# Optimization experiments

Hardware: AMD Instinct MI355X
Metric: run time of the kernel (lower is better)

The kernel has to match this reference:

```python
import jax, jax.numpy as jnp
import numpy as np

B, T, V, E, U, L = 64, 1024, 512, 256, 512, 3


def setup_inputs() -> dict:
    key = jax.random.key(0)
    ks = jax.random.split(key, 16)
    inp = {}
    inp['tokens'] = jax.random.randint(ks[0], (B, T), 0, V)
    inp['lengths'] = jax.random.randint(ks[1], (B,), 1, T + 1)
    inp['emb'] = jax.random.normal(ks[2], (V, E), jnp.float32) * 0.05
    in_dims = [E, U, U]
    for l in range(L):
        inp[f'Wk{l}'] = jax.random.normal(ks[3 + 3 * l], (in_dims[l], 4 * U), jnp.float32) * 0.05
        inp[f'Wr{l}'] = jax.random.normal(ks[4 + 3 * l], (U, 4 * U), jnp.float32) * 0.05
        # Keras unit_forget_bias: forget-gate bias initialized to 1
        b = jnp.zeros((4 * U,), jnp.float32)
        inp[f'b{l}'] = b.at[U:2 * U].set(1.0)
    inp['Wd'] = jax.random.normal(ks[12], (U, V), jnp.float32) * 0.05
    inp['bd'] = jnp.zeros((V,), jnp.float32)
    return inp


def _lstm_layer(x_tm, mask_tm, Wk, Wr, b):
    # x_tm: [T,B,D] time-major, mask_tm: [T,B] bool
    Bb = x_tm.shape[1]
    Uu = Wr.shape[0]
    h0 = jnp.zeros((Bb, Uu), x_tm.dtype)
    c0 = jnp.zeros((Bb, Uu), x_tm.dtype)

    def step(carry, inp):
        h, c = carry
        xt, mt = inp
        z = xt @ Wk + h @ Wr + b  # [B, 4U]
        i, f, g, o = jnp.split(z, 4, axis=-1)
        i = jax.nn.sigmoid(i)
        f = jax.nn.sigmoid(f)
        g = jnp.tanh(g)
        o = jax.nn.sigmoid(o)
        c_new = f * c + i * g
        h_new = o * jnp.tanh(c_new)
        m = mt[:, None]
        # masked steps: carry previous state, emit zeros (zero_output_for_mask=True)
        h2 = jnp.where(m, h_new, h)
        c2 = jnp.where(m, c_new, c)
        out = jnp.where(m, h_new, jnp.zeros_like(h_new))
        return (h2, c2), out

    _, ys = jax.lax.scan(step, (h0, c0), (x_tm, mask_tm))
    return ys  # [T,B,U]


def reference(tokens, lengths, emb, Wk0, Wr0, b0, Wk1, Wr1, b1, Wk2, Wr2, b2, Wd, bd):
    Tt = tokens.shape[1]
    mask = jnp.arange(Tt)[None, :] < lengths[:, None]  # [B,T], sequence_mask
    x = emb[tokens]  # [B,T,E] embedding lookup
    x = jnp.swapaxes(x, 0, 1)  # time-major [T,B,E]
    m = jnp.swapaxes(mask, 0, 1)  # [T,B]
    for Wk, Wr, b in ((Wk0, Wr0, b0), (Wk1, Wr1, b1), (Wk2, Wr2, b2)):
        x = _lstm_layer(x, m, Wk, Wr, b)
    x = jnp.swapaxes(x, 0, 1)  # [B,T,U]
    logits = x @ Wd + bd  # [B,T,V]
    return logits
```

## Files before the change

kernel.cpp:

```cpp
#include <hip/hip_runtime.h>
#include <stdint.h>

typedef unsigned short u16;
typedef unsigned int   u32;
typedef unsigned long long u64;
typedef _Float16 half8 __attribute__((ext_vector_type(8)));
typedef __attribute__((ext_vector_type(4))) float f32x4;

#define DEV static __device__ __forceinline__

DEV float bf2f(u16 u){ union{u32 i; float f;} v; v.i=((u32)u)<<16; return v.f; }
DEV u16 f2bf(float f){ u32 x=__float_as_uint(f); return (u16)((x + 0x7FFFu + ((x>>16)&1u))>>16); }
DEV u16 f2hu(float f){ _Float16 h = (_Float16)f; return *(u16*)&h; }
DEV float hu2f(u16 u){ _Float16 h = *(_Float16*)&u; return (float)h; }
DEV float sigm(float x){ return 1.0f/(1.0f+__expf(-x)); }
DEV float tanhr(float x){ float a=fabsf(x); float e=__expf(-2.0f*a); float t=(1.0f-e)/(1.0f+e); return x<0.0f? -t:t; }

typedef const __attribute__((address_space(1))) u32 gu32;
typedef __attribute__((address_space(3))) u32 lu32;
DEV void gload16(const void* g, void* l){
  __builtin_amdgcn_global_load_lds((gu32*)g, (lu32*)l, 16, 0, 0);
}
DEV void gstore4c(void* p, u32 v){
  asm volatile("global_store_dword %0, %1, off sc0 sc1" : : "v"(p), "v"(v) : "memory");
}

DEV u16 ld_h(const void* p, size_t i, int isbf){
  float f = isbf ? bf2f(((const u16*)p)[i]) : ((const float*)p)[i];
  return f2hu(f);
}

__global__ void detect_dtype(const void* emb, u32* flag)
{
  const u16* p = (const u16*)emb;
  int i = threadIdx.x;
  u32 e0 = (p[i]    >> 7) & 0xFF;
  u32 e1 = (p[i+64] >> 7) & 0xFF;
  unsigned long long b0 = __ballot(e0 >= 0x60 && e0 <= 0x7E);
  unsigned long long b1 = __ballot(e1 >= 0x60 && e1 <= 0x7E);
  if (i == 0) *flag = (__popcll(b0) + __popcll(b1) > 96) ? 1u : 0u;
}

__global__ __launch_bounds__(256) void embconv(const void* __restrict__ emb, u16* __restrict__ embH,
                                               const u32* __restrict__ flag)
{
  const int isbf = *flag;
  int i = blockIdx.x*256 + threadIdx.x;
  embH[i] = ld_h(emb, i, isbf);
}

__global__ __launch_bounds__(256) void transpose_bt(const void* __restrict__ in,
                                                    u16* __restrict__ out,
                                                    int K, int N, int perm,
                                                    const u32* __restrict__ flag)
{
  const int isbf = *flag;
  __shared__ u16 t[32][33];
  int nb = blockIdx.x*32, kb = blockIdx.y*32;
  int tx = threadIdx.x & 31, ty = threadIdx.x >> 5;
  #pragma unroll
  for (int i=0;i<4;++i){
    int kl = ty + i*8;
    t[kl][tx] = ld_h(in, (size_t)(kb+kl)*N + nb + tx, isbf);
  }
  __syncthreads();
  #pragma unroll
  for (int i=0;i<4;++i){
    int nl = ty + i*8;
    int n = nb + nl;
    int np = perm ? ((n & 511)*4 + (n >> 9)) : n;
    out[(size_t)np*K + kb + tx] = t[tx][nl];
  }
}

__global__ __launch_bounds__(256) void bias_prep(const void* __restrict__ in, float* __restrict__ out,
                                                 int N, int perm, const u32* __restrict__ flag)
{
  const int isbf = *flag;
  int n = blockIdx.x*256 + threadIdx.x;
  if (n < N){
    int np = perm ? ((n & 511)*4 + (n >> 9)) : n;
    out[np] = isbf ? bf2f(((const u16*)in)[n]) : ((const float*)in)[n];
  }
}

__global__ __launch_bounds__(256) void gemm3(
    const u16* __restrict__ A1, const u16* __restrict__ A2,
    const u16* __restrict__ BT0, const u16* __restrict__ BT1, const u16* __restrict__ BT2,
    const float* __restrict__ b0p, const float* __restrict__ b1p, const float* __restrict__ b2p,
    u16* __restrict__ C0, u16* __restrict__ C1, u16* __restrict__ C2,
    const int* __restrict__ tok, const u16* __restrict__ embH, int t0g,
    int act0, int act1, int act2)
{
  const int z = blockIdx.z;
  if (z==0 && !act0) return;
  if (z==1 && !act1) return;
  if (z==2 && !act2) return;
  const int K = (z==0) ? 256 : 512;
  const u16* BT = z==0?BT0 : z==1?BT1 : BT2;
  const float* bias = z==0?b0p : z==1?b1p : b2p;
  u16* C = z==0?C0 : z==1?C1 : C2;

  __shared__ u16 As[128*32];
  __shared__ u16 Bs[128*32];
  const int tid = threadIdx.x, lane = tid & 63, wid = tid >> 6;
  const int wr = wid >> 1, wc = wid & 1;
  const int m0 = blockIdx.x*128, n0 = blockIdx.y*128;
  const int r  = tid >> 2;
  const int ce = (tid & 3)*8;
  const u16 *a0, *a1;
  if (z == 0){
    int r0 = m0 + r;     int tt = t0g + (r0>>6); int bb = r0 & 63;
    a0 = embH + (size_t)tok[bb*1024 + tt]*256 + ce;
    int r1 = m0 + 64 + r; tt = t0g + (r1>>6); bb = r1 & 63;
    a1 = embH + (size_t)tok[bb*1024 + tt]*256 + ce;
  } else {
    const u16* A = (z==1) ? A1 : A2;
    a0 = A + (size_t)(m0 + r)*512 + ce;
    a1 = A + (size_t)(m0 + 64 + r)*512 + ce;
  }
  const u16* bp0 = BT + (size_t)(n0 + r)*K + ce;
  const u16* bp1 = BT + (size_t)(n0 + 64 + r)*K + ce;
  char* asw0 = (char*)As + (wid<<10);
  char* asw1 = (char*)As + 4096 + (wid<<10);
  char* bsw0 = (char*)Bs + (wid<<10);
  char* bsw1 = (char*)Bs + 4096 + (wid<<10);

  f32x4 acc[4][4];
  #pragma unroll
  for (int i=0;i<4;++i)
    #pragma unroll
    for (int j=0;j<4;++j) acc[i][j] = (f32x4){0.f,0.f,0.f,0.f};

  const int koff = (lane>>4)*8;
  for (int k0 = 0; k0 < K; k0 += 32){
    __syncthreads();
    gload16(a0 + k0, asw0);
    gload16(a1 + k0, asw1);
    gload16(bp0 + k0, bsw0);
    gload16(bp1 + k0, bsw1);
    __syncthreads();
    half8 af[4], bf[4];
    #pragma unroll
    for (int mt=0;mt<4;++mt) af[mt] = *(const half8*)(As + (wr*64 + mt*16 + (lane&15))*32 + koff);
    #pragma unroll
    for (int nt=0;nt<4;++nt) bf[nt] = *(const half8*)(Bs + (wc*64 + nt*16 + (lane&15))*32 + koff);
    #pragma unroll
    for (int mt=0;mt<4;++mt)
      #pragma unroll
      for (int nt=0;nt<4;++nt)
        acc[mt][nt] = __builtin_amdgcn_mfma_f32_16x16x32_f16(bf[nt], af[mt], acc[mt][nt], 0,0,0);
  }
  #pragma unroll
  for (int mt=0;mt<4;++mt){
    int m = m0 + wr*64 + mt*16 + (lane&15);
    int ltl = m >> 6, b = m & 63;
    #pragma unroll
    for (int nt=0;nt<4;++nt){
      int u = ((n0 + wc*64 + nt*16) >> 2) + (lane>>4);
      float4 bq = *(const float4*)(bias + u*4);
      u16 qo[4];
      qo[0] = f2hu(acc[mt][nt][0] + bq.x);
      qo[1] = f2hu(acc[mt][nt][1] + bq.y);
      qo[2] = f2hu(acc[mt][nt][2] + bq.z);
      qo[3] = f2hu(acc[mt][nt][3] + bq.w);
      ((uint2*)C)[(size_t)(ltl*512 + u)*64 + b] = *(uint2*)qo;
    }
  }
}

__global__ __launch_bounds__(256) void gemm_bt(const u16* __restrict__ A, const u16* __restrict__ BT,
                                               const float* __restrict__ bias, void* __restrict__ C,
                                               int M, int N, int K, const u32* __restrict__ flag)
{
  __shared__ u16 As[128*32];
  __shared__ u16 Bs[128*32];
  const int tid = threadIdx.x, lane = tid & 63, wid = tid >> 6;
  const int wr = wid >> 1, wc = wid & 1;
  const int m0 = blockIdx.x*128, n0 = blockIdx.y*128;
  const int r  = tid >> 2;
  const int ce = (tid & 3)*8;
  const u16* a0 = A  + (size_t)(m0 + r)*K + ce;
  const u16* a1 = A  + (size_t)(m0 + 64 + r)*K + ce;
  const u16* b0 = BT + (size_t)(n0 + r)*K + ce;
  const u16* b1 = BT + (size_t)(n0 + 64 + r)*K + ce;
  char* asw0 = (char*)As + (wid<<10);
  char* asw1 = (char*)As + 4096 + (wid<<10);
  char* bsw0 = (char*)Bs + (wid<<10);
  char* bsw1 = (char*)Bs + 4096 + (wid<<10);

  f32x4 acc[4][4];
  #pragma unroll
  for (int i=0;i<4;++i)
    #pragma unroll
    for (int j=0;j<4;++j) acc[i][j] = (f32x4){0.f,0.f,0.f,0.f};

  const int koff = (lane>>4)*8;
  for (int k0 = 0; k0 < K; k0 += 32){
    __syncthreads();
    gload16(a0 + k0, asw0);
    gload16(a1 + k0, asw1);
    gload16(b0 + k0, bsw0);
    gload16(b1 + k0, bsw1);
    __syncthreads();
    half8 af[4], bf[4];
    #pragma unroll
    for (int mt=0;mt<4;++mt) af[mt] = *(const half8*)(As + (wr*64 + mt*16 + (lane&15))*32 + koff);
    #pragma unroll
    for (int nt=0;nt<4;++nt) bf[nt] = *(const half8*)(Bs + (wc*64 + nt*16 + (lane&15))*32 + koff);
    #pragma unroll
    for (int mt=0;mt<4;++mt)
      #pragma unroll
      for (int nt=0;nt<4;++nt)
        acc[mt][nt] = __builtin_amdgcn_mfma_f32_16x16x32_f16(af[mt], bf[nt], acc[mt][nt], 0,0,0);
  }
  const int wrf32 = (*flag == 0);
  #pragma unroll
  for (int mt=0;mt<4;++mt){
    #pragma unroll
    for (int nt=0;nt<4;++nt){
      int col = n0 + wc*64 + nt*16 + (lane&15);
      float bv = bias[col];
      #pragma unroll
      for (int j=0;j<4;++j){
        int row = m0 + wr*64 + mt*16 + ((lane>>4)<<2) + j;
        int orow = ((row & 63) << 10) | (row >> 6);
        float v = acc[mt][nt][j] + bv;
        if (wrf32) ((float*)C)[(size_t)orow*N + col] = v;
        else       ((u16*)C)[(size_t)orow*N + col] = f2bf(v);
      }
    }
  }
}

__global__ __launch_bounds__(256,1) void lstm3(
    const uint2* __restrict__ Zq0, const uint2* __restrict__ Zq1, const uint2* __restrict__ Zq2,
    const u16* __restrict__ Wr0T, const u16* __restrict__ Wr1T, const u16* __restrict__ Wr2T,
    const int* __restrict__ lengths,
    u16* __restrict__ xo0, u16* __restrict__ xo1, u16* __restrict__ xf,
    u32* Hbase, float* Cbase, int d)
{
  __shared__ char Hs[16384];
  const int tid = threadIdx.x, lane = tid & 63, w = tid >> 6;
  const int layer = blockIdx.x >> 6;
  const int sub = blockIdx.x & 63;
  const int g = sub >> 4, i = sub & 15;
  const int c = d - layer;
  if (c < 0 || c > 15) return;
  const int t0 = c * 64;

  const uint2* Zq = layer==0?Zq0 : layer==1?Zq1 : Zq2;
  const u16* WrT  = layer==0?Wr0T : layer==1?Wr1T : Wr2T;
  u32* Hb0 = Hbase + (size_t)layer*65536;
  u32* Hb1 = Hb0 + 32768;
  float* Cg = Cbase + (size_t)layer*32768;

  const int q = lane >> 4, r15 = lane & 15, rsw = r15 & 7;
  const int bglob = g*16 + r15;
  const int mylen = lengths[bglob];
  const int u0 = i*32 + w*8 + q;
  const int u1 = u0 + 4;

  half8 wreg[2][16];
  #pragma unroll
  for (int mt=0; mt<2; ++mt){
    const u16* wsrc = WrT + (size_t)(i*128 + (w*2+mt)*16 + r15)*512 + q*8;
    #pragma unroll
    for (int kk=0; kk<16; ++kk)
      wreg[mt][kk] = *(const half8*)(wsrc + kk*32);
  }
  float c0 = Cg[bglob*512 + u0];
  float c1 = Cg[bglob*512 + u1];

  int chrow[4], chblk[4];
  #pragma unroll
  for (int jj=0;jj<4;++jj){ int ch = jj*256 + tid; chrow[jj] = ch>>6; chblk[jj] = ch & 63; }

  for (int lt = 0; lt < 64; ++lt){
    const int t = t0 + lt;
    u32* Hcur = (t & 1) ? Hb1 : Hb0;
    u32* Hnxt = (t & 1) ? Hb0 : Hb1;

    uint2 zqa = Zq[(size_t)(lt*512 + u0)*64 + bglob];
    uint2 zqb = Zq[(size_t)(lt*512 + u1)*64 + bglob];

    {
      const u32 tg = (u32)t;
      u32 pend = 0xF;
      do {
        #pragma unroll
        for (int jj=0;jj<4;++jj) if (pend & (1u<<jj)){
          const u64* src = (const u64*)(Hcur + (size_t)(g*16 + chrow[jj])*512 + chblk[jj]*8);
          u64 a0 = __hip_atomic_load(src+0, __ATOMIC_RELAXED, __HIP_MEMORY_SCOPE_AGENT);
          u64 a1 = __hip_atomic_load(src+1, __ATOMIC_RELAXED, __HIP_MEMORY_SCOPE_AGENT);
          u64 a2 = __hip_atomic_load(src+2, __ATOMIC_RELAXED, __HIP_MEMORY_SCOPE_AGENT);
          u64 a3 = __hip_atomic_load(src+3, __ATOMIC_RELAXED, __HIP_MEMORY_SCOPE_AGENT);
          bool ok = (((u32)a0)>>16)==tg && (((u32)(a0>>32))>>16)==tg
                 && (((u32)a1)>>16)==tg && (((u32)(a1>>32))>>16)==tg
                 && (((u32)a2)>>16)==tg && (((u32)(a2>>32))>>16)==tg
                 && (((u32)a3)>>16)==tg && (((u32)(a3>>32))>>16)==tg;
          if (ok){
            uint4 v;
            v.x = (((u32)a0)&0xFFFFu) | (((u32)(a0>>32))<<16);
            v.y = (((u32)a1)&0xFFFFu) | (((u32)(a1>>32))<<16);
            v.z = (((u32)a2)&0xFFFFu) | (((u32)(a2>>32))<<16);
            v.w = (((u32)a3)&0xFFFFu) | (((u32)(a3>>32))<<16);
            *(uint4*)(Hs + chrow[jj]*1024 + ((chblk[jj] ^ (chrow[jj] & 7))<<4)) = v;
            pend &= ~(1u<<jj);
          }
        }
      } while (pend);
    }
    __syncthreads();

    f32x4 acc0 = {0.f,0.f,0.f,0.f}, acc1 = {0.f,0.f,0.f,0.f};
    #pragma unroll
    for (int kk=0;kk<16;++kk){
      half8 hf = *(const half8*)(Hs + r15*1024 + (((kk*4 + q) ^ rsw)<<4));
      acc0 = __builtin_amdgcn_mfma_f32_16x16x32_f16(wreg[0][kk], hf, acc0, 0,0,0);
      acc1 = __builtin_amdgcn_mfma_f32_16x16x32_f16(wreg[1][kk], hf, acc1, 0,0,0);
    }

    const bool live = t < mylen;
    u16 hst0, hst1, xv0, xv1;
    {
      float zi = hu2f((u16)zqa.x)        + acc0[0];
      float zf = hu2f((u16)(zqa.x>>16))  + acc0[1];
      float zg = hu2f((u16)zqa.y)        + acc0[2];
      float zo = hu2f((u16)(zqa.y>>16))  + acc0[3];
      float ii = sigm(zi), ff = sigm(zf), gg = tanhr(zg), oo = sigm(zo);
      float cn = ff*c0 + ii*gg;
      float hn = oo*tanhr(cn);
      c0 = live ? cn : c0;
      int ub = u0*2;
      float hold = hu2f(*(const u16*)(Hs + r15*1024 + (((ub>>4) ^ rsw)<<4) + (ub & 15)));
      hst0 = f2hu(live ? hn : hold);
      xv0  = f2hu(live ? hn : 0.f);
    }
    {
      float zi = hu2f((u16)zqb.x)        + acc1[0];
      float zf = hu2f((u16)(zqb.x>>16))  + acc1[1];
      float zg = hu2f((u16)zqb.y)        + acc1[2];
      float zo = hu2f((u16)(zqb.y>>16))  + acc1[3];
      float ii = sigm(zi), ff = sigm(zf), gg = tanhr(zg), oo = sigm(zo);
      float cn = ff*c1 + ii*gg;
      float hn = oo*tanhr(cn);
      c1 = live ? cn : c1;
      int ub = u1*2;
      float hold = hu2f(*(const u16*)(Hs + r15*1024 + (((ub>>4) ^ rsw)<<4) + (ub & 15)));
      hst1 = f2hu(live ? hn : hold);
      xv1  = f2hu(live ? hn : 0.f);
    }
    u32 s0 = (((u32)(t+1))<<16) | (u32)hst0;
    u32 s1 = (((u32)(t+1))<<16) | (u32)hst1;
    gstore4c(Hnxt + (size_t)bglob*512 + u0, s0);
    gstore4c(Hnxt + (size_t)bglob*512 + u1, s1);
    if (layer == 2){
      xf[((size_t)t*64 + bglob)*512 + u0] = xv0;
      xf[((size_t)t*64 + bglob)*512 + u1] = xv1;
    } else {
      u16* xo = layer ? xo1 : xo0;
      xo[((size_t)lt*64 + bglob)*512 + u0] = xv0;
      xo[((size_t)lt*64 + bglob)*512 + u1] = xv1;
    }
    __syncthreads();
  }
  Cg[bglob*512 + u0] = c0;
  Cg[bglob*512 + u1] = c1;
}

extern "C" void kernel_launch(void* const* d_in, const int* in_sizes, int n_in,
                              void* d_out, int out_size, void* d_ws, size_t ws_size,
                              hipStream_t stream)
{
  const int* tokens  = (const int*)d_in[0];
  const int* lengths = (const int*)d_in[1];
  const void* emb    = d_in[2];
  const void* Wk[3] = {d_in[3], d_in[6], d_in[9]};
  const void* Wr[3] = {d_in[4], d_in[7], d_in[10]};
  const void* bv[3] = {d_in[5], d_in[8], d_in[11]};
  const void* Wd = d_in[12];
  const void* bd = d_in[13];

  char* ws = (char*)d_ws;
  size_t o = 0;
  u16* Zq0 = (u16*)(ws+o); o += 16777216;
  u16* Zq1 = (u16*)(ws+o); o += 16777216;
  u16* Zq2 = (u16*)(ws+o); o += 16777216;
  u16* xo0 = (u16*)(ws+o); o += 4096ull*512*2;
  u16* xo1 = (u16*)(ws+o); o += 4096ull*512*2;
  u16* xf  = (u16*)(ws+o); o += 65536ull*512*2;
  u16* embH = (u16*)(ws+o); o += 512ull*256*2;
  u16* WkT0 = (u16*)(ws+o); o += 2048ull*256*2;
  u16* WkT1 = (u16*)(ws+o); o += 2048ull*512*2;
  u16* WkT2 = (u16*)(ws+o); o += 2048ull*512*2;
  u16* WrT[3];
  for (int l=0;l<3;++l){ WrT[l] = (u16*)(ws+o); o += 2048ull*512*2; }
  u16* WdT = (u16*)(ws+o); o += 512ull*512*2;
  float* biasP[3];
  for (int l=0;l<3;++l){ biasP[l] = (float*)(ws+o); o += 2048*4; }
  float* bdP = (float*)(ws+o); o += 512*4;
  size_t ctrl0 = o;
  u32*  Hbase = (u32*)(ws+o); o += 3ull*65536*4;
  float* Cbase = (float*)(ws+o); o += 3ull*32768*4;
  u32* dtypeflag = (u32*)(ws+o); o += 256;
  size_t need = o;
  if (ws_size < need) return;

  hipMemsetAsync(ws + ctrl0, 0, need - ctrl0, stream);

  detect_dtype<<<1,64,0,stream>>>(emb, dtypeflag);
  embconv<<<512,256,0,stream>>>(emb, embH, dtypeflag);
  transpose_bt<<<dim3(64,8) ,256,0,stream>>>(Wk[0], WkT0, 256, 2048, 1, dtypeflag);
  transpose_bt<<<dim3(64,16),256,0,stream>>>(Wk[1], WkT1, 512, 2048, 1, dtypeflag);
  transpose_bt<<<dim3(64,16),256,0,stream>>>(Wk[2], WkT2, 512, 2048, 1, dtypeflag);
  for (int l=0;l<3;++l)
    transpose_bt<<<dim3(64,16),256,0,stream>>>(Wr[l], WrT[l], 512, 2048, 1, dtypeflag);
  transpose_bt<<<dim3(16,16),256,0,stream>>>(Wd, WdT, 512, 512, 0, dtypeflag);
  for (int l=0;l<3;++l) bias_prep<<<8,256,0,stream>>>(bv[l], biasP[l], 2048, 1, dtypeflag);
  bias_prep<<<2,256,0,stream>>>(bd, bdP, 512, 0, dtypeflag);

  for (int d=0; d<18; ++d){
    int act0 = (d <= 15);
    int act1 = (d >= 1 && d <= 16);
    int act2 = (d >= 2);
    gemm3<<<dim3(32,16,3),256,0,stream>>>(xo0, xo1, WkT0, WkT1, WkT2,
                                          biasP[0], biasP[1], biasP[2],
                                          Zq0, Zq1, Zq2,
                                          tokens, embH, d*64, act0, act1, act2);
    lstm3<<<192,256,0,stream>>>((const uint2*)Zq0, (const uint2*)Zq1, (const uint2*)Zq2,
                                WrT[0], WrT[1], WrT[2],
                                lengths, xo0, xo1, xf, Hbase, Cbase, d);
  }
  gemm_bt<<<dim3(512,4),256,0,stream>>>(xf, WdT, bdP, d_out, 65536, 512, 512, dtypeflag);
}
```

Baseline: 5.206 ms.

## Double LSTM block threads, double-buffer LDS hidden state, drop trailing barrier

The recurrent LSTM kernel now runs 512 threads per block, so each wave owns one 16-row MFMA tile instead of two. This halves per-thread weight registers and gate work on the serial critical path. The hidden-state staging buffer in LDS is double-buffered by step parity so the end-of-step __syncthreads can be removed. The spin-wait poll now uses inline dwordx4 cache-bypassing loads with an s_sleep backoff in place of 64-bit atomic loads. Risks are more barrier cost with 8 waves and extra polling latency from the sleep.

```diff
diff --git a/kernel.cpp b/kernel.cpp
--- a/kernel.cpp
+++ b/kernel.cpp
@@ -233,14 +233,14 @@
   }
 }
 
-__global__ __launch_bounds__(256,1) void lstm3(
+__global__ __launch_bounds__(512,2) void lstm3(
     const uint2* __restrict__ Zq0, const uint2* __restrict__ Zq1, const uint2* __restrict__ Zq2,
     const u16* __restrict__ Wr0T, const u16* __restrict__ Wr1T, const u16* __restrict__ Wr2T,
     const int* __restrict__ lengths,
     u16* __restrict__ xo0, u16* __restrict__ xo1, u16* __restrict__ xf,
     u32* Hbase, float* Cbase, int d)
 {
-  __shared__ char Hs[16384];
+  __shared__ char Hs[2][16384];
   const int tid = threadIdx.x, lane = tid & 63, w = tid >> 6;
   const int layer = blockIdx.x >> 6;
   const int sub = blockIdx.x & 63;
@@ -258,115 +258,104 @@
   const int q = lane >> 4, r15 = lane & 15, rsw = r15 & 7;
   const int bglob = g*16 + r15;
   const int mylen = lengths[bglob];
-  const int u0 = i*32 + w*8 + q;
-  const int u1 = u0 + 4;
-
-  half8 wreg[2][16];
-  #pragma unroll
-  for (int mt=0; mt<2; ++mt){
-    const u16* wsrc = WrT + (size_t)(i*128 + (w*2+mt)*16 + r15)*512 + q*8;
+  const int u0 = i*32 + w*4 + q;
+
+  half8 wreg[16];
+  {
+    const u16* wsrc = WrT + (size_t)(i*128 + w*16 + r15)*512 + q*8;
     #pragma unroll
     for (int kk=0; kk<16; ++kk)
-      wreg[mt][kk] = *(const half8*)(wsrc + kk*32);
+      wreg[kk] = *(const half8*)(wsrc + kk*32);
   }
   float c0 = Cg[bglob*512 + u0];
-  float c1 = Cg[bglob*512 + u1];
-
-  int chrow[4], chblk[4];
-  #pragma unroll
-  for (int jj=0;jj<4;++jj){ int ch = jj*256 + tid; chrow[jj] = ch>>6; chblk[jj] = ch & 63; }
+
+  const int ch0 = tid*2, ch1 = tid*2 + 1;
+  const int row0 = ch0 >> 6, blk0 = ch0 & 63;
+  const int row1 = ch1 >> 6, blk1 = ch1 & 63;
+  const int so0 = row0*1024 + ((blk0 ^ (row0 & 7))<<4);
+  const int so1 = row1*1024 + ((blk1 ^ (row1 & 7))<<4);
 
   for (int lt = 0; lt < 64; ++lt){
     const int t = t0 + lt;
     u32* Hcur = (t & 1) ? Hb1 : Hb0;
     u32* Hnxt = (t & 1) ? Hb0 : Hb1;
+    char* Hsb = Hs[lt & 1];
 
     uint2 zqa = Zq[(size_t)(lt*512 + u0)*64 + bglob];
-    uint2 zqb = Zq[(size_t)(lt*512 + u1)*64 + bglob];
 
     {
       const u32 tg = (u32)t;
-      u32 pend = 0xF;
+      const u32* p0 = Hcur + (size_t)(g*16 + row0)*512 + blk0*8;
+      const u32* p1 = Hcur + (size_t)(g*16 + row1)*512 + blk1*8;
+      u32 pend = 3;
       do {
-        #pragma unroll
-        for (int jj=0;jj<4;++jj) if (pend & (1u<<jj)){
-          const u64* src = (const u64*)(Hcur + (size_t)(g*16 + chrow[jj])*512 + chblk[jj]*8);
-          u64 a0 = __hip_atomic_load(src+0, __ATOMIC_RELAXED, __HIP_MEMORY_SCOPE_AGENT);
-          u64 a1 = __hip_atomic_load(src+1, __ATOMIC_RELAXED, __HIP_MEMORY_SCOPE_AGENT);
-          u64 a2 = __hip_atomic_load(src+2, __ATOMIC_RELAXED, __HIP_MEMORY_SCOPE_AGENT);
-          u64 a3 = __hip_atomic_load(src+3, __ATOMIC_RELAXED, __HIP_MEMORY_SCOPE_AGENT);
-          bool ok = (((u32)a0)>>16)==tg && (((u32)(a0>>32))>>16)==tg
-                 && (((u32)a1)>>16)==tg && (((u32)(a1>>32))>>16)==tg
-                 && (((u32)a2)>>16)==tg && (((u32)(a2>>32))>>16)==tg
-                 && (((u32)a3)>>16)==tg && (((u32)(a3>>32))>>16)==tg;
+        uint4 va, vb, vc, vd;
+        asm volatile(
+          "global_load_dwordx4 %0, %4, off sc0 sc1\n\t"
+          "global_load_dwordx4 %1, %5, off sc0 sc1\n\t"
+          "global_load_dwordx4 %2, %6, off sc0 sc1\n\t"
+          "global_load_dwordx4 %3, %7, off sc0 sc1\n\t"
+          "s_waitcnt vmcnt(0)"
+          : "=&v"(va), "=&v"(vb), "=&v"(vc), "=&v"(vd)
+          : "v"(p0), "v"((const u32*)(p0+4)), "v"(p1), "v"((const u32*)(p1+4))
+          : "memory");
+        if (pend & 1u){
+          bool ok = (va.x>>16)==tg && (va.y>>16)==tg && (va.z>>16)==tg && (va.w>>16)==tg
+                 && (vb.x>>16)==tg && (vb.y>>16)==tg && (vb.z>>16)==tg && (vb.w>>16)==tg;
           if (ok){
-            uint4 v;
-            v.x = (((u32)a0)&0xFFFFu) | (((u32)(a0>>32))<<16);
-            v.y = (((u32)a1)&0xFFFFu) | (((u32)(a1>>32))<<16);
-            v.z = (((u32)a2)&0xFFFFu) | (((u32)(a2>>32))<<16);
-            v.w = (((u32)a3)&0xFFFFu) | (((u32)(a3>>32))<<16);
-            *(uint4*)(Hs + chrow[jj]*1024 + ((chblk[jj] ^ (chrow[jj] & 7))<<4)) = v;
-            pend &= ~(1u<<jj);
+            uint4 o;
+            o.x = (va.x&0xFFFFu)|(va.y<<16); o.y = (va.z&0xFFFFu)|(va.w<<16);
+            o.z = (vb.x&0xFFFFu)|(vb.y<<16); o.w = (vb.z&0xFFFFu)|(vb.w<<16);
+            *(uint4*)(Hsb + so0) = o;
+            pend &= ~1u;
           }
         }
+        if (pend & 2u){
+          bool ok = (vc.x>>16)==tg && (vc.y>>16)==tg && (vc.z>>16)==tg && (vc.w>>16)==tg
+                 && (vd.x>>16)==tg && (vd.y>>16)==tg && (vd.z>>16)==tg && (vd.w>>16)==tg;
+          if (ok){
+            uint4 o;
+            o.x = (vc.x&0xFFFFu)|(vc.y<<16); o.y = (vc.z&0xFFFFu)|(vc.w<<16);
+            o.z = (vd.x&0xFFFFu)|(vd.y<<16); o.w = (vd.z&0xFFFFu)|(vd.w<<16);
+            *(uint4*)(Hsb + so1) = o;
+            pend &= ~2u;
+          }
+        }
+        if (pend) __builtin_amdgcn_s_sleep(1);
       } while (pend);
     }
     __syncthreads();
 
-    f32x4 acc0 = {0.f,0.f,0.f,0.f}, acc1 = {0.f,0.f,0.f,0.f};
+    f32x4 acc = {0.f,0.f,0.f,0.f};
     #pragma unroll
     for (int kk=0;kk<16;++kk){
-      half8 hf = *(const half8*)(Hs + r15*1024 + (((kk*4 + q) ^ rsw)<<4));
-      acc0 = __builtin_amdgcn_mfma_f32_16x16x32_f16(wreg[0][kk], hf, acc0, 0,0,0);
-      acc1 = __builtin_amdgcn_mfma_f32_16x16x32_f16(wreg[1][kk], hf, acc1, 0,0,0);
+      half8 hf = *(const half8*)(Hsb + r15*1024 + (((kk*4 + q) ^ rsw)<<4));
+      acc = __builtin_amdgcn_mfma_f32_16x16x32_f16(wreg[kk], hf, acc, 0,0,0);
     }
 
     const bool live = t < mylen;
-    u16 hst0, hst1, xv0, xv1;
-    {
-      float zi = hu2f((u16)zqa.x)        + acc0[0];
-      float zf = hu2f((u16)(zqa.x>>16))  + acc0[1];
-      float zg = hu2f((u16)zqa.y)        + acc0[2];
-      float zo = hu2f((u16)(zqa.y>>16))  + acc0[3];
-      float ii = sigm(zi), ff = sigm(zf), gg = tanhr(zg), oo = sigm(zo);
-      float cn = ff*c0 + ii*gg;
-      float hn = oo*tanhr(cn);
-      c0 = live ? cn : c0;
-      int ub = u0*2;
-      float hold = hu2f(*(const u16*)(Hs + r15*1024 + (((ub>>4) ^ rsw)<<4) + (ub & 15)));
-      hst0 = f2hu(live ? hn : hold);
-      xv0  = f2hu(live ? hn : 0.f);
+    float zi = hu2f((u16)zqa.x)        + acc[0];
+    float zf = hu2f((u16)(zqa.x>>16))  + acc[1];
+    float zg = hu2f((u16)zqa.y)        + acc[2];
+    float zo = hu2f((u16)(zqa.y>>16))  + acc[3];
+    float ii = sigm(zi), ff = sigm(zf), gg = tanhr(zg), oo = sigm(zo);
+    float cn = ff*c0 + ii*gg;
+    float hn = oo*tanhr(cn);
+    c0 = live ? cn : c0;
+    int ub = u0*2;
+    float hold = hu2f(*(const u16*)(Hsb + r15*1024 + (((ub>>4) ^ rsw)<<4) + (ub & 15)));
+    u16 hst = f2hu(live ? hn : hold);
+    u16 xv  = f2hu(live ? hn : 0.f);
+
+    gstore4c(Hnxt + (size_t)bglob*512 + u0, (((u32)(t+1))<<16) | (u32)hst);
+    if (layer == 2)
+      xf[((size_t)t*64 + bglob)*512 + u0] = xv;
+    else {
+      u16* xo = layer ? xo1 : xo0;
+      xo[((size_t)lt*64 + bglob)*512 + u0] = xv;
     }
-    {
-      float zi = hu2f((u16)zqb.x)        + acc1[0];
-      float zf = hu2f((u16)(zqb.x>>16))  + acc1[1];
-      float zg = hu2f((u16)zqb.y)        + acc1[2];
-      float zo = hu2f((u16)(zqb.y>>16))  + acc1[3];
-      float ii = sigm(zi), ff = sigm(zf), gg = tanhr(zg), oo = sigm(zo);
-      float cn = ff*c1 + ii*gg;
-      float hn = oo*tanhr(cn);
-      c1 = live ? cn : c1;
-      int ub = u1*2;
-      float hold = hu2f(*(const u16*)(Hs + r15*1024 + (((ub>>4) ^ rsw)<<4) + (ub & 15)));
-      hst1 = f2hu(live ? hn : hold);
-      xv1  = f2hu(live ? hn : 0.f);
-    }
-    u32 s0 = (((u32)(t+1))<<16) | (u32)hst0;
-    u32 s1 = (((u32)(t+1))<<16) | (u32)hst1;
-    gstore4c(Hnxt + (size_t)bglob*512 + u0, s0);
-    gstore4c(Hnxt + (size_t)bglob*512 + u1, s1);
-    if (layer == 2){
-      xf[((size_t)t*64 + bglob)*512 + u0] = xv0;
-      xf[((size_t)t*64 + bglob)*512 + u1] = xv1;
-    } else {
-      u16* xo = layer ? xo1 : xo0;
-      xo[((size_t)lt*64 + bglob)*512 + u0] = xv0;
-      xo[((size_t)lt*64 + bglob)*512 + u1] = xv1;
-    }
-    __syncthreads();
   }
   Cg[bglob*512 + u0] = c0;
-  Cg[bglob*512 + u1] = c1;
 }
 
 extern "C" void kernel_launch(void* const* d_in, const int* in_sizes, int n_in,
@@ -428,7 +417,7 @@
                                           biasP[0], biasP[1], biasP[2],
                                           Zq0, Zq1, Zq2,
                                           tokens, embH, d*64, act0, act1, act2);
-    lstm3<<<192,256,0,stream>>>((const uint2*)Zq0, (const uint2*)Zq1, (const uint2*)Zq2,
+    lstm3<<<192,512,0,stream>>>((const uint2*)Zq0, (const uint2*)Zq1, (const uint2*)Zq2,
                                 WrT[0], WrT[1], WrT[2],
                                 lengths, xo0, xo1, xf, Hbase, Cbase, d);
   }
```

After: 7.081 ms. 1.36x slower.
